# Kernel optimization log

Measured on AMD Instinct MI355X. Metric: run time of the kernel, lower is better.

Reference implementation:

```python
import jax, jax.numpy as jnp
import numpy as np
from jax import lax

EPS = 1e-10

def _safe_norm(x):
    # torch remove_zeros: replace exact-zero norms with 1e-10
    n = jnp.linalg.norm(x, axis=-1, keepdims=True)
    return jnp.where(n != 0, n, jnp.full_like(n, EPS))

def setup_inputs() -> dict:
    key = jax.random.key(0)
    ks = jax.random.split(key, 5)
    S, B, D = 2048, 32, 512  # seq, batch, 2*hidden
    K = 147  # odd(max_entries/14)
    return {
        "encoder_outputs": jax.random.normal(ks[0], (S, B, D), dtype=jnp.float32),
        "state": jax.random.normal(ks[1], (B, D), dtype=jnp.float32),
        "previous_attention": jax.random.uniform(ks[2], (B, S), dtype=jnp.float32),
        "W_att": jax.random.normal(ks[3], (D, D), dtype=jnp.float32) / np.sqrt(D),
        "b_att": jax.random.normal(ks[4], (D,), dtype=jnp.float32) * 0.01,
        "conv_w": jnp.ones((1, 1, K), dtype=jnp.float32),
        "conv_b": jnp.zeros((1,), dtype=jnp.float32),
    }

def reference(encoder_outputs, state, previous_attention, W_att, b_att, conv_w, conv_b):
    S, B, D = encoder_outputs.shape
    # attended state via linear layer, then cosine-similarity weights (vectorized over seq)
    attended = state @ W_att.T + b_att                       # [B, D]
    ns = attended / _safe_norm(attended)                     # [B, D]
    ne = encoder_outputs / _safe_norm(encoder_outputs)       # [S, B, D]
    weights = jnp.einsum('bd,sbd->bs', ns, ne)               # [B, S]
    # conv1d time smoothing of previous attention (same-length, odd kernel)
    k = conv_w.shape[-1]
    pad = k // 2
    y = lax.conv_general_dilated(previous_attention[:, None, :], conv_w,
                                 window_strides=(1,), padding=[(pad, pad)])
    adjusted = jax.nn.relu(y[:, 0, :] + conv_b)              # [B, S]
    prev_probs = adjusted / jnp.sum(adjusted, axis=1, keepdims=True)
    adj = prev_probs * jax.nn.softmax(weights, axis=1)
    norm_w = adj / jnp.sum(adj, axis=1, keepdims=True)       # [B, S]
    applied = jnp.einsum('bs,sbd->bd', norm_w, encoder_outputs)  # [B, D]
    return applied, norm_w
```

## Files before the change

### kernel.cpp

```cpp
#include <hip/hip_runtime.h>
#include <hip/hip_bf16.h>
#include <math.h>


__device__ __forceinline__ float wave_sum(float v) {
    for (int off = 32; off; off >>= 1) v += __shfl_xor(v, off);
    return v;
}

__global__ __launch_bounds__(256) void front_kernel(
    const float* __restrict__ state, const float* __restrict__ W,
    const float* __restrict__ bias, const float* __restrict__ prev,
    const float* __restrict__ cw, const float* __restrict__ cb,
    float* __restrict__ attended, float* __restrict__ adj,
    int S, int D, int K) {
    __shared__ __align__(16) float smem[1024];
    int b = blockIdx.y;
    int t = threadIdx.x;

    if (blockIdx.x < 2) {
        if (t < D / 4)
            ((float4*)smem)[t] = ((const float4*)(state + (size_t)b * D))[t];
        __syncthreads();
        int d = blockIdx.x * 256 + t;
        const float4* Wrow = (const float4*)(W + (size_t)d * D);
        const float4* sv = (const float4*)smem;
        float acc = bias[d];
#pragma unroll 8
        for (int k = 0; k < 128; ++k) {
            float4 w4 = Wrow[k];
            float4 s4 = sv[k];
            acc += w4.x * s4.x + w4.y * s4.y + w4.z * s4.z + w4.w * s4.w;
        }
        attended[(size_t)b * D + d] = acc;
    } else {
        int s0 = (blockIdx.x - 2) * 256;
        int pad = K / 2;
        int seglen = 256 + K - 1;
        float* seg = smem;
        float* wk = smem + 512;
        for (int i = t; i < seglen; i += 256) {
            int s = s0 - pad + i;
            seg[i] = (s >= 0 && s < S) ? prev[(size_t)b * S + s] : 0.f;
        }
        for (int j = t; j < K; j += 256) wk[j] = cw[j];
        __syncthreads();
        float y = cb[0];
        for (int j = 0; j < K; ++j) y += seg[t + j] * wk[j];
        adj[(size_t)b * S + s0 + t] = fmaxf(y, 0.f);
    }
}

__global__ __launch_bounds__(256) void main_kernel(
    const float* __restrict__ e, const float* __restrict__ attended,
    const float* __restrict__ adj, float* __restrict__ partial,
    float* __restrict__ zbuf, float* __restrict__ u,
    int S, int B, int D, int CH) {
    int wave = threadIdx.x >> 6;
    int lane = threadIdx.x & 63;
    int c = blockIdx.x * 4 + wave;
    int b = blockIdx.y;

    const float4* att4 = (const float4*)(attended + (size_t)b * D);
    float4 a0 = att4[lane];
    float4 a1 = att4[lane + 64];
    float asq = a0.x * a0.x + a0.y * a0.y + a0.z * a0.z + a0.w * a0.w
              + a1.x * a1.x + a1.y * a1.y + a1.z * a1.z + a1.w * a1.w;
    asq = wave_sum(asq);
    float an = sqrtf(asq);
    if (an == 0.f) an = 1e-10f;
    float ainv = 1.f / an;
    float4 ns0, ns1;
    ns0.x = a0.x * ainv; ns0.y = a0.y * ainv; ns0.z = a0.z * ainv; ns0.w = a0.w * ainv;
    ns1.x = a1.x * ainv; ns1.y = a1.y * ainv; ns1.z = a1.z * ainv; ns1.w = a1.w * ainv;

    float4 acc0 = {0.f, 0.f, 0.f, 0.f};
    float4 acc1 = {0.f, 0.f, 0.f, 0.f};
    float z = 0.f;

    int s0 = c * CH;
    const float4* row4 = (const float4*)(e + ((size_t)s0 * B + b) * D);
    size_t rstride = (size_t)B * D / 4;

    float4 x0 = row4[lane];
    float4 x1 = row4[lane + 64];
    for (int i = 0; i < CH; ++i) {
        float4 nx0, nx1;
        if (i + 1 < CH) {
            nx0 = row4[rstride + lane];
            nx1 = row4[rstride + lane + 64];
        }
        float dot = x0.x * ns0.x + x0.y * ns0.y + x0.z * ns0.z + x0.w * ns0.w
                  + x1.x * ns1.x + x1.y * ns1.y + x1.z * ns1.z + x1.w * ns1.w;
        float sq  = x0.x * x0.x + x0.y * x0.y + x0.z * x0.z + x0.w * x0.w
                  + x1.x * x1.x + x1.y * x1.y + x1.z * x1.z + x1.w * x1.w;
        dot = wave_sum(dot);
        sq  = wave_sum(sq);
        float n = sqrtf(sq);
        if (n == 0.f) n = 1e-10f;
        float w = dot / n;
        float coef = adj[(size_t)b * S + s0 + i] * __expf(w);
        if (lane == 0) u[(size_t)b * S + s0 + i] = coef;
        acc0.x += coef * x0.x; acc0.y += coef * x0.y;
        acc0.z += coef * x0.z; acc0.w += coef * x0.w;
        acc1.x += coef * x1.x; acc1.y += coef * x1.y;
        acc1.z += coef * x1.z; acc1.w += coef * x1.w;
        z += coef;
        x0 = nx0; x1 = nx1;
        row4 += rstride;
    }

    float4* p4 = (float4*)(partial + ((size_t)c * B + b) * D);
    p4[lane] = acc0;
    p4[lane + 64] = acc1;
    if (lane == 0) zbuf[(size_t)c * B + b] = z;
}

__global__ __launch_bounds__(256) void combine_kernel(
    const float* __restrict__ partial, const float* __restrict__ zbuf,
    const float* __restrict__ u, float* __restrict__ applied,
    float* __restrict__ norm_w, int S, int B, int D, int NCB) {
    int b = blockIdx.x;
    int t = threadIdx.x;
    int lane = t & 63, wv = t >> 6;
    __shared__ float red[4];
    __shared__ float zsh;

    float zt = (t < NCB) ? zbuf[(size_t)t * B + b] : 0.f;
    zt = wave_sum(zt);
    if (lane == 0) red[wv] = zt;
    __syncthreads();
    if (t == 0) zsh = 1.f / (red[0] + red[1] + red[2] + red[3]);
    __syncthreads();
    float inv = zsh;

    if (t < D / 4) {
        float4 acc = {0.f, 0.f, 0.f, 0.f};
        const float4* p4 = (const float4*)partial;
        for (int cix = 0; cix < NCB; ++cix) {
            float4 x = p4[((size_t)cix * B + b) * (D / 4) + t];
            acc.x += x.x; acc.y += x.y; acc.z += x.z; acc.w += x.w;
        }
        acc.x *= inv; acc.y *= inv; acc.z *= inv; acc.w *= inv;
        ((float4*)(applied + (size_t)b * D))[t] = acc;
    }

    for (int s = t; s < S; s += 256)
        norm_w[(size_t)b * S + s] = u[(size_t)b * S + s] * inv;
}

extern "C" void kernel_launch(void* const* d_in, const int* in_sizes, int n_in,
                              void* d_out, int out_size, void* d_ws, size_t ws_size,
                              hipStream_t stream) {
    const float* enc   = (const float*)d_in[0];
    const float* state = (const float*)d_in[1];
    const float* prev  = (const float*)d_in[2];
    const float* W     = (const float*)d_in[3];
    const float* bias  = (const float*)d_in[4];
    const float* cw    = (const float*)d_in[5];
    const float* cb    = (const float*)d_in[6];

    const int S = in_sizes[0] / in_sizes[1];
    const int B = in_sizes[2] / S;
    const int D = in_sizes[1] / B;
    const int K = in_sizes[5];

    float* out     = (float*)d_out;
    float* applied = out;
    float* norm_w  = out + (size_t)B * D;

    const int NCB = 128;
    const int CH = S / NCB;

    float* ws       = (float*)d_ws;
    float* attended = ws;
    float* adj      = attended + (size_t)B * D;
    float* u        = adj + (size_t)B * S;
    float* zbuf     = u + (size_t)B * S;
    float* partial  = zbuf + (size_t)NCB * B;

    front_kernel<<<dim3(2 + S / 256, B), 256, 0, stream>>>(
        state, W, bias, prev, cw, cb, attended, adj, S, D, K);
    main_kernel<<<dim3(NCB / 4, B), 256, 0, stream>>>(
        enc, attended, adj, partial, zbuf, u, S, B, D, CH);
    combine_kernel<<<B, 256, 0, stream>>>(
        partial, zbuf, u, applied, norm_w, S, B, D, NCB);
}
```

Baseline: 250.6 us.

## Reduce partials in-block via LDS and parallelize combine across D slices

The main kernel now sums the four per-wave partial accumulators in shared memory before writing, so partial-buffer traffic drops by a factor of four. It also loads the adj values for a chunk once per lane and broadcasts them with shuffles instead of issuing a scalar load each iteration. The combine kernel becomes a 2D grid of four blocks per batch, each reducing a slice of D over 32 partials with a two-stage shared-memory reduction and writing a quarter of norm_w with float4 stores. The cost is an extra LDS buffer and a __syncthreads in main_kernel, and combine_kernel assumes S=2048, D=512 and 32 partials.

```diff
diff --git a/kernel.cpp b/kernel.cpp
--- a/kernel.cpp
+++ b/kernel.cpp
@@ -1,5 +1,4 @@
 #include <hip/hip_runtime.h>
-#include <hip/hip_bf16.h>
 #include <math.h>
 
 
@@ -56,6 +55,7 @@
     const float* __restrict__ adj, float* __restrict__ partial,
     float* __restrict__ zbuf, float* __restrict__ u,
     int S, int B, int D, int CH) {
+    __shared__ __align__(16) float reds[4 * 512 + 4];
     int wave = threadIdx.x >> 6;
     int lane = threadIdx.x & 63;
     int c = blockIdx.x * 4 + wave;
@@ -74,11 +74,15 @@
     ns0.x = a0.x * ainv; ns0.y = a0.y * ainv; ns0.z = a0.z * ainv; ns0.w = a0.w * ainv;
     ns1.x = a1.x * ainv; ns1.y = a1.y * ainv; ns1.z = a1.z * ainv; ns1.w = a1.w * ainv;
 
+    int s0 = c * CH;
+
+    float adjv = 0.f;
+    if (CH <= 64 && lane < CH) adjv = adj[(size_t)b * S + s0 + lane];
+
     float4 acc0 = {0.f, 0.f, 0.f, 0.f};
     float4 acc1 = {0.f, 0.f, 0.f, 0.f};
     float z = 0.f;
 
-    int s0 = c * CH;
     const float4* row4 = (const float4*)(e + ((size_t)s0 * B + b) * D);
     size_t rstride = (size_t)B * D / 4;
 
@@ -99,7 +103,8 @@
         float n = sqrtf(sq);
         if (n == 0.f) n = 1e-10f;
         float w = dot / n;
-        float coef = adj[(size_t)b * S + s0 + i] * __expf(w);
+        float av = (CH <= 64) ? __shfl(adjv, i) : adj[(size_t)b * S + s0 + i];
+        float coef = av * __expf(w);
         if (lane == 0) u[(size_t)b * S + s0 + i] = coef;
         acc0.x += coef * x0.x; acc0.y += coef * x0.y;
         acc0.z += coef * x0.z; acc0.w += coef * x0.w;
@@ -110,43 +115,76 @@
         row4 += rstride;
     }
 
-    float4* p4 = (float4*)(partial + ((size_t)c * B + b) * D);
-    p4[lane] = acc0;
-    p4[lane + 64] = acc1;
-    if (lane == 0) zbuf[(size_t)c * B + b] = z;
+    float* wsl = reds + (wave << 9);
+    ((float4*)wsl)[lane] = acc0;
+    ((float4*)wsl)[lane + 64] = acc1;
+    if (lane == 0) reds[2048 + wave] = z;
+    __syncthreads();
+    int t = threadIdx.x;
+    if (t < 128) {
+        const float4* r4 = (const float4*)reds;
+        float4 v0 = r4[t];
+        float4 v1 = r4[t + 128];
+        float4 v2 = r4[t + 256];
+        float4 v3 = r4[t + 384];
+        float4 o;
+        o.x = v0.x + v1.x + v2.x + v3.x;
+        o.y = v0.y + v1.y + v2.y + v3.y;
+        o.z = v0.z + v1.z + v2.z + v3.z;
+        o.w = v0.w + v1.w + v2.w + v3.w;
+        ((float4*)(partial + ((size_t)blockIdx.x * B + b) * D))[t] = o;
+    }
+    if (t == 0)
+        zbuf[(size_t)blockIdx.x * B + b] =
+            reds[2048] + reds[2049] + reds[2050] + reds[2051];
 }
 
 __global__ __launch_bounds__(256) void combine_kernel(
     const float* __restrict__ partial, const float* __restrict__ zbuf,
     const float* __restrict__ u, float* __restrict__ applied,
-    float* __restrict__ norm_w, int S, int B, int D, int NCB) {
-    int b = blockIdx.x;
+    float* __restrict__ norm_w, int S, int B, int D, int NPART) {
+    int q = blockIdx.x;
+    int b = blockIdx.y;
     int t = threadIdx.x;
-    int lane = t & 63, wv = t >> 6;
-    __shared__ float red[4];
+    __shared__ __align__(16) float4 red4[8][32];
     __shared__ float zsh;
 
-    float zt = (t < NCB) ? zbuf[(size_t)t * B + b] : 0.f;
+    float zt = (t < NPART) ? zbuf[(size_t)t * B + b] : 0.f;
     zt = wave_sum(zt);
-    if (lane == 0) red[wv] = zt;
-    __syncthreads();
-    if (t == 0) zsh = 1.f / (red[0] + red[1] + red[2] + red[3]);
+    if (t == 0) zsh = 1.f / zt;
+
+    int c2 = t >> 5;
+    int di = t & 31;
+    int d4 = q * 32 + di;
+    const float4* p4 = (const float4*)partial;
+    float4 a = {0.f, 0.f, 0.f, 0.f};
+#pragma unroll
+    for (int k = 0; k < 4; ++k) {
+        float4 x = p4[((size_t)(c2 + (k << 3)) * B + b) * (D >> 2) + d4];
+        a.x += x.x; a.y += x.y; a.z += x.z; a.w += x.w;
+    }
+    red4[c2][di] = a;
     __syncthreads();
     float inv = zsh;
-
-    if (t < D / 4) {
-        float4 acc = {0.f, 0.f, 0.f, 0.f};
-        const float4* p4 = (const float4*)partial;
-        for (int cix = 0; cix < NCB; ++cix) {
-            float4 x = p4[((size_t)cix * B + b) * (D / 4) + t];
-            acc.x += x.x; acc.y += x.y; acc.z += x.z; acc.w += x.w;
-        }
-        acc.x *= inv; acc.y *= inv; acc.z *= inv; acc.w *= inv;
-        ((float4*)(applied + (size_t)b * D))[t] = acc;
-    }
-
-    for (int s = t; s < S; s += 256)
-        norm_w[(size_t)b * S + s] = u[(size_t)b * S + s] * inv;
+    if (t < 32) {
+        float4 s = red4[0][t];
+#pragma unroll
+        for (int j = 1; j < 8; ++j) {
+            float4 x = red4[j][t];
+            s.x += x.x; s.y += x.y; s.z += x.z; s.w += x.w;
+        }
+        s.x *= inv; s.y *= inv; s.z *= inv; s.w *= inv;
+        ((float4*)(applied + (size_t)b * D))[q * 32 + t] = s;
+    }
+
+    const float4* u4 = (const float4*)(u + (size_t)b * S);
+    float4* nw4 = (float4*)(norm_w + (size_t)b * S);
+    if (t < 128) {
+        int idx = q * (S >> 4) + t;
+        float4 x = u4[idx];
+        x.x *= inv; x.y *= inv; x.z *= inv; x.w *= inv;
+        nw4[idx] = x;
+    }
 }
 
 extern "C" void kernel_launch(void* const* d_in, const int* in_sizes, int n_in,
@@ -169,20 +207,21 @@
     float* applied = out;
     float* norm_w  = out + (size_t)B * D;
 
-    const int NCB = 128;
-    const int CH = S / NCB;
+    const int NCHUNK = 128;
+    const int CH = S / NCHUNK;
+    const int NPART = NCHUNK / 4;
 
     float* ws       = (float*)d_ws;
     float* attended = ws;
     float* adj      = attended + (size_t)B * D;
     float* u        = adj + (size_t)B * S;
     float* zbuf     = u + (size_t)B * S;
-    float* partial  = zbuf + (size_t)NCB * B;
+    float* partial  = zbuf + (size_t)NPART * B;
 
     front_kernel<<<dim3(2 + S / 256, B), 256, 0, stream>>>(
         state, W, bias, prev, cw, cb, attended, adj, S, D, K);
-    main_kernel<<<dim3(NCB / 4, B), 256, 0, stream>>>(
+    main_kernel<<<dim3(NPART, B), 256, 0, stream>>>(
         enc, attended, adj, partial, zbuf, u, S, B, D, CH);
-    combine_kernel<<<B, 256, 0, stream>>>(
-        partial, zbuf, u, applied, norm_w, S, B, D, NCB);
-}
+    combine_kernel<<<dim3(4, B), 256, 0, stream>>>(
+        partial, zbuf, u, applied, norm_w, S, B, D, NPART);
+}
```

Result: faster. 220.0 us (-12.2%).
